# Kernel optimization log

Measured on AMD Instinct MI355X. Metric: run time of the kernel, lower is better.

The kernel has to match this reference:

```python
import jax, jax.numpy as jnp
import numpy as np

EMBED = 256
HEADS = 8
LEVELS = 4
POINTS = 4
HD = EMBED // HEADS  # 32
SHAPES = [(100, 100), (50, 50), (25, 25), (13, 13)]  # (H, W) per level
NV = sum(h * w for h, w in SHAPES)  # 13294
BS = 2


def _lin_params(k, fan_in, fan_out):
    s = 1.0 / np.sqrt(fan_in)
    kw, kb = jax.random.split(k)
    W = jax.random.uniform(kw, (fan_in, fan_out), jnp.float32, -s, s)
    b = jax.random.uniform(kb, (fan_out,), jnp.float32, -s, s)
    return W, b


def setup_inputs():
    key = jax.random.key(0)
    ks = jax.random.split(key, 10)
    inp = {
        "query": jax.random.normal(ks[0], (BS, NV, EMBED), jnp.float32),
        "key": jax.random.normal(ks[1], (BS, NV, EMBED), jnp.float32),
        "value": jax.random.normal(ks[2], (BS, NV, EMBED), jnp.float32),
        "query_pos": jax.random.normal(ks[3], (BS, NV, EMBED), jnp.float32),
        "reference_points": jax.random.uniform(ks[4], (BS, NV, LEVELS, 2), jnp.float32),
        "spatial_shapes": jnp.array(SHAPES, jnp.int32),
        "level_start_index": jnp.array(np.cumsum([0] + [h * w for h, w in SHAPES[:-1]]), jnp.int32),
        "key_padding_mask": jnp.zeros((BS, NV), bool),
    }
    inp["W_value"], inp["b_value"] = _lin_params(ks[5], EMBED, EMBED)
    inp["W_off"], inp["b_off"] = _lin_params(ks[6], EMBED, HEADS * LEVELS * POINTS * 2)
    inp["W_attn"], inp["b_attn"] = _lin_params(ks[7], EMBED, HEADS * LEVELS * POINTS)
    inp["W_out"], inp["b_out"] = _lin_params(ks[8], EMBED, EMBED)
    inp["W_ffn"], inp["b_ffn"] = _lin_params(ks[9], EMBED, EMBED)
    return inp


def _bilinear(v, x, y, H, W):
    # v: (bs, heads, H*W, hd); x, y: (bs, heads, n) pixel coords (align_corners=False)
    # zero padding outside the feature map (matches torch grid_sample padding_mode='zeros')
    x0 = jnp.floor(x)
    y0 = jnp.floor(y)
    lx = x - x0
    ly = y - y0
    x0 = x0.astype(jnp.int32)
    y0 = y0.astype(jnp.int32)

    def g(xi, yi):
        valid = ((xi >= 0) & (xi < W) & (yi >= 0) & (yi < H)).astype(v.dtype)
        idx = jnp.clip(yi, 0, H - 1) * W + jnp.clip(xi, 0, W - 1)
        return jnp.take_along_axis(v, idx[..., None], axis=2) * valid[..., None]

    return (g(x0, y0) * ((1 - lx) * (1 - ly))[..., None]
            + g(x0 + 1, y0) * (lx * (1 - ly))[..., None]
            + g(x0, y0 + 1) * ((1 - lx) * ly)[..., None]
            + g(x0 + 1, y0 + 1) * (lx * ly)[..., None])


def _forward(query, key, value, query_pos, reference_points, shapes, starts,
             key_padding_mask, W_value, b_value, W_off, b_off, W_attn, b_attn,
             W_out, b_out, W_ffn, b_ffn):
    bs, nq, _ = query.shape
    identity = query  # residual taken BEFORE adding positional encoding (mmcv semantics)
    q = query + query_pos
    v = value @ W_value + b_value
    v = jnp.where(key_padding_mask[..., None], 0.0, v).reshape(bs, -1, HEADS, HD)
    off = (q @ W_off + b_off).reshape(bs, nq, HEADS, LEVELS, POINTS, 2)
    aw = jax.nn.softmax((q @ W_attn + b_attn).reshape(bs, nq, HEADS, LEVELS * POINTS), axis=-1)
    aw = aw.reshape(bs, nq, HEADS, LEVELS, POINTS)
    # offset normalizer is (W, H) per level
    wh = jnp.array([[w, h] for h, w in shapes], jnp.float32)
    loc = reference_points[:, :, None, :, None, :] + off / wh[None, None, None, :, None, :]
    out = jnp.zeros((bs, HEADS, nq, HD), q.dtype)
    for l, (H, W) in enumerate(shapes):
        s = starts[l]
        vl = v[:, s:s + H * W].transpose(0, 2, 1, 3)  # (bs, heads, H*W, hd)
        x = (loc[:, :, :, l, :, 0] * W - 0.5).transpose(0, 2, 1, 3).reshape(bs, HEADS, nq * POINTS)
        y = (loc[:, :, :, l, :, 1] * H - 0.5).transpose(0, 2, 1, 3).reshape(bs, HEADS, nq * POINTS)
        smp = _bilinear(vl, x, y, H, W).reshape(bs, HEADS, nq, POINTS, HD)
        wl = aw[:, :, :, l].transpose(0, 2, 1, 3)  # (bs, heads, nq, P)
        out = out + jnp.sum(smp * wl[..., None], axis=3)
    out = out.transpose(0, 2, 1, 3).reshape(bs, nq, EMBED)
    out = out @ W_out + b_out + identity
    return out @ W_ffn + b_ffn


def reference(query, key, value, query_pos, reference_points, spatial_shapes,
              level_start_index, key_padding_mask, W_value, b_value, W_off, b_off,
              W_attn, b_attn, W_out, b_out, W_ffn, b_ffn):
    # spatial shapes / level starts are structural metadata -> treat as static ints
    shapes = [tuple(int(x) for x in r) for r in np.asarray(spatial_shapes)]
    starts = [int(x) for x in np.asarray(level_start_index)]
    return _forward(query, key, value, query_pos, reference_points, shapes, starts,
                    key_padding_mask, W_value, b_value, W_off, b_off, W_attn, b_attn,
                    W_out, b_out, W_ffn, b_ffn)
```

## Files before the change

### kernel.cpp

```cpp
#include <hip/hip_runtime.h>
#include <hip/hip_bf16.h>
#include <math.h>

#define NQ 13294
#define NV 13294
#define M_ROWS (2*NQ)
#define MP 26624

typedef __attribute__((ext_vector_type(8))) short bf16x8;
typedef __attribute__((ext_vector_type(4))) float f32x4;

__device__ __forceinline__ float4 ld4(const float* p){ return *(const float4*)p; }
__device__ __forceinline__ float bfu_lo(unsigned int u){ return __uint_as_float(u << 16); }
__device__ __forceinline__ float bfu_hi(unsigned int u){ return __uint_as_float(u & 0xffff0000u); }
__device__ __forceinline__ unsigned short f2bf(float f){
  unsigned int u = __float_as_uint(f);
  u += 0x7fffu + ((u >> 16) & 1u);
  return (unsigned short)(u >> 16);
}
__device__ __forceinline__ unsigned int pk2(float a, float b){
  return (unsigned int)f2bf(a) | ((unsigned int)f2bf(b) << 16);
}
__device__ __forceinline__ void gl_lds16(const unsigned short* g, unsigned short* l) {
  __builtin_amdgcn_global_load_lds(
      (const __attribute__((address_space(1))) unsigned int*)g,
      (__attribute__((address_space(3))) unsigned int*)l, 16, 0, 0);
}

__global__ __launch_bounds__(256) void prep_all(
    const float* __restrict__ value, const float* __restrict__ query,
    const float* __restrict__ qpos,
    unsigned short* __restrict__ val_bf, unsigned short* __restrict__ q_bf,
    const float* __restrict__ wv, const float* __restrict__ wo,
    const float* __restrict__ wa, const float* __restrict__ wu,
    const float* __restrict__ wf, unsigned short* __restrict__ wt)
{
  const int total = MP * 64;
  for (int i = blockIdx.x * 256 + threadIdx.x; i < total; i += gridDim.x * 256) {
    const int e = i * 4;
    ushort4 a = make_ushort4(0,0,0,0), b = make_ushort4(0,0,0,0);
    if (e < M_ROWS * 256) {
      float4 v4 = ld4(value + e);
      a = make_ushort4(f2bf(v4.x), f2bf(v4.y), f2bf(v4.z), f2bf(v4.w));
      float4 q4 = ld4(query + e);
      float4 p4 = ld4(qpos + e);
      b = make_ushort4(f2bf(q4.x+p4.x), f2bf(q4.y+p4.y), f2bf(q4.z+p4.z), f2bf(q4.w+p4.w));
    }
    *(ushort4*)(val_bf + e) = a;
    *(ushort4*)(q_bf   + e) = b;
  }
  for (int t = blockIdx.x * 256 + threadIdx.x; t < 294912; t += gridDim.x * 256) {
    const float* src; int Nn; int base;
    if      (t < 65536)  { src = wv; Nn = 256; base = 0; }
    else if (t < 131072) { src = wo; Nn = 256; base = 65536; }
    else if (t < 163840) { src = wa; Nn = 128; base = 131072; }
    else if (t < 229376) { src = wu; Nn = 256; base = 163840; }
    else                 { src = wf; Nn = 256; base = 229376; }
    const int local = t - base;
    const int n = local >> 8, k = local & 255;
    wt[t] = f2bf(src[k * Nn + n]);
  }
}

template<int NCOL, int OUT_MODE, bool ADD_RES>
__global__ __launch_bounds__(256) void gemm_gl(
    const unsigned short* __restrict__ A, const unsigned short* __restrict__ Bt,
    const float* __restrict__ biasA, const float* __restrict__ biasB,
    const float* __restrict__ RES, void* __restrict__ Cv, int N)
{
  __shared__ unsigned short lds[32768];

  const int nwg = 416 * NCOL;
  const int lin = blockIdx.x;
  const int swz = (lin & 7) * (nwg >> 3) + (lin >> 3);
  const int brow = (swz / NCOL) * 64;
  const int bcol = (swz % NCOL) * 64;

  const int tid  = threadIdx.x;
  const int wid  = tid >> 6, lane = tid & 63;
  const int wr   = wid >> 1, wc = wid & 1;
  const int fr   = lane & 15, fg = lane >> 4;

  {
    const int r0   = lane >> 3;
    const int slot = lane & 7;
    #pragma unroll
    for (int t = 0; t < 4; ++t) {
      #pragma unroll
      for (int c = 0; c < 2; ++c) {
        const int row = (wid * 2 + c) * 8 + r0;
        const int gsl = slot ^ (row & 7);
        gl_lds16(A  + (size_t)(brow + row) * 256 + t * 64 + (gsl << 3),
                 &lds[t * 4096 + (wid * 2 + c) * 512]);
        gl_lds16(Bt + (size_t)(bcol + row) * 256 + t * 64 + (gsl << 3),
                 &lds[16384 + t * 4096 + (wid * 2 + c) * 512]);
      }
    }
  }
  __syncthreads();

  f32x4 acc[2][2];
  #pragma unroll
  for (int m = 0; m < 2; ++m)
    #pragma unroll
    for (int n = 0; n < 2; ++n)
      acc[m][n] = (f32x4){0.f, 0.f, 0.f, 0.f};

  #pragma unroll
  for (int t = 0; t < 4; ++t) {
    const char* as = (const char*)&lds[t * 4096];
    const char* bs = (const char*)&lds[16384 + t * 4096];
    #pragma unroll
    for (int kk = 0; kk < 2; ++kk) {
      const int kb = kk * 64 + fg * 16;
      bf16x8 af[2], bfv[2];
      #pragma unroll
      for (int m = 0; m < 2; ++m) {
        const int r = wr * 32 + m * 16 + fr;
        af[m] = *(const bf16x8*)(as + r * 128 + (kb ^ ((r & 7) << 4)));
      }
      #pragma unroll
      for (int n = 0; n < 2; ++n) {
        const int r = wc * 32 + n * 16 + fr;
        bfv[n] = *(const bf16x8*)(bs + r * 128 + (kb ^ ((r & 7) << 4)));
      }
      #pragma unroll
      for (int m = 0; m < 2; ++m)
        #pragma unroll
        for (int n = 0; n < 2; ++n)
          acc[m][n] = __builtin_amdgcn_mfma_f32_16x16x32_bf16(af[m], bfv[n], acc[m][n], 0, 0, 0);
    }
  }

  __syncthreads();
  float* csh = (float*)lds;
  const int c0 = bcol + wc * 32 + fr;
  const int c1 = c0 + 16;
  const float bn0 = (c0 < 256) ? biasA[c0] : biasB[c0 - 256];
  const float bn1 = (c1 < 256) ? biasA[c1] : biasB[c1 - 256];
  #pragma unroll
  for (int m = 0; m < 2; ++m)
    #pragma unroll
    for (int j = 0; j < 4; ++j) {
      const int row = wr * 32 + m * 16 + fg * 4 + j;
      csh[row * 64 + wc * 32 + fr]      = acc[m][0][j] + bn0;
      csh[row * 64 + wc * 32 + 16 + fr] = acc[m][1][j] + bn1;
    }
  __syncthreads();
  #pragma unroll
  for (int i = 0; i < 4; ++i) {
    const int rl = i * 16 + (tid >> 4);
    const int gr = brow + rl;
    if (gr >= M_ROWS) continue;
    const int c4 = (tid & 15) * 4;
    float4 v = *(const float4*)&csh[rl * 64 + c4];
    if (ADD_RES) {
      float4 q = ld4(RES + (size_t)gr * 256 + bcol + c4);
      v.x += q.x; v.y += q.y; v.z += q.z; v.w += q.w;
    }
    if (OUT_MODE == 0) {
      *(float4*)&((float*)Cv)[(size_t)gr * N + bcol + c4] = v;
    } else if (OUT_MODE == 1) {
      ushort4 pk = make_ushort4(f2bf(v.x), f2bf(v.y), f2bf(v.z), f2bf(v.w));
      *(ushort4*)&((unsigned short*)Cv)[(size_t)gr * N + bcol + c4] = pk;
    } else {
      const int head = (bcol + c4) >> 5;
      const int ch   = c4 & 31;
      ushort4 pk = make_ushort4(f2bf(v.x), f2bf(v.y), f2bf(v.z), f2bf(v.w));
      *(ushort4*)&((unsigned short*)Cv)[((size_t)head * M_ROWS + gr) * 32 + ch] = pk;
    }
  }
}

__global__ __launch_bounds__(256) void msda5(
    const unsigned short* __restrict__ v, const unsigned short* __restrict__ oa,
    const float* __restrict__ ref, unsigned short* __restrict__ attout)
{
  constexpr int LW[4] = {100, 50, 25, 13};
  constexpr int LS[4] = {0, 10000, 12500, 13125};

  __shared__ int4   sidx[64][16];
  __shared__ float4 swt [64][16];

  const int bid   = blockIdx.x;
  const int h     = bid & 7;
  const int chunk = bid >> 3;
  const int tid   = threadIdx.x;
  const int qi    = tid >> 2;
  const int lq    = tid & 3;
  const int bq    = chunk * 64 + qi;
  const bool active = bq < M_ROWS;
  const int b     = (bq >= NQ) ? 1 : 0;
  const int pmask = qi & 7;

  if (active) {
    const int l = lq;
    const int W = LW[l];
    const float fD = (float)W;
    const unsigned short* oarow = oa + (size_t)bq * 384;

    uint2 lg = *(const uint2*)(oarow + 256 + h * 16 + l * 4);
    float g0 = bfu_lo(lg.x), g1 = bfu_hi(lg.x), g2 = bfu_lo(lg.y), g3 = bfu_hi(lg.y);
    float mx = fmaxf(fmaxf(g0, g1), fmaxf(g2, g3));
    mx = fmaxf(mx, __shfl_xor(mx, 1));
    mx = fmaxf(mx, __shfl_xor(mx, 2));
    float e0 = __expf(g0-mx), e1 = __expf(g1-mx), e2 = __expf(g2-mx), e3 = __expf(g3-mx);
    float s = e0 + e1 + e2 + e3;
    s += __shfl_xor(s, 1);
    s += __shfl_xor(s, 2);
    const float inv = 1.f / s;
    const float ee[4] = {e0*inv, e1*inv, e2*inv, e3*inv};

    uint4 ov = *(const uint4*)(oarow + h * 32 + l * 8);
    const float oxy[8] = {bfu_lo(ov.x), bfu_hi(ov.x), bfu_lo(ov.y), bfu_hi(ov.y),
                          bfu_lo(ov.z), bfu_hi(ov.z), bfu_lo(ov.w), bfu_hi(ov.w)};
    const float rx = ref[(size_t)bq * 8 + l * 2];
    const float ry = ref[(size_t)bq * 8 + l * 2 + 1];
    const int rowbase = b * NV + LS[l];

    #pragma unroll
    for (int j = 0; j < 4; ++j) {
      const float x = (rx + oxy[2*j]   / fD) * fD - 0.5f;
      const float y = (ry + oxy[2*j+1] / fD) * fD - 0.5f;
      const float x0f = floorf(x), y0f = floorf(y);
      const float lx = x - x0f, ly = y - y0f;
      const int x0 = (int)x0f, y0 = (int)y0f;
      const int x1 = x0 + 1,  y1 = y0 + 1;
      const int cx0 = min(max(x0, 0), W - 1), cx1 = min(max(x1, 0), W - 1);
      const int cy0 = min(max(y0, 0), W - 1), cy1 = min(max(y1, 0), W - 1);
      const float f00 = (x0 >= 0 && x0 < W && y0 >= 0 && y0 < W) ? 1.f : 0.f;
      const float f10 = (x1 >= 0 && x1 < W && y0 >= 0 && y0 < W) ? 1.f : 0.f;
      const float f01 = (x0 >= 0 && x0 < W && y1 >= 0 && y1 < W) ? 1.f : 0.f;
      const float f11 = (x1 >= 0 && x1 < W && y1 >= 0 && y1 < W) ? 1.f : 0.f;
      const float wt = ee[j];
      const int pi = (l * 4 + j) ^ pmask;
      sidx[qi][pi] = make_int4((rowbase + cy0 * W + cx0) * 64,
                               (rowbase + cy0 * W + cx1) * 64,
                               (rowbase + cy1 * W + cx0) * 64,
                               (rowbase + cy1 * W + cx1) * 64);
      swt[qi][pi] = make_float4(wt * (1.f - lx) * (1.f - ly) * f00,
                                wt * lx * (1.f - ly) * f10,
                                wt * (1.f - lx) * ly * f01,
                                wt * lx * ly * f11);
    }
  }
  __syncthreads();

  if (active) {
    const char* vb = (const char*)v + (size_t)h * M_ROWS * 64 + lq * 16;
    float acc[8] = {0.f, 0.f, 0.f, 0.f, 0.f, 0.f, 0.f, 0.f};
    #pragma unroll
    for (int p = 0; p < 16; ++p) {
      const int4   ix = sidx[qi][p ^ pmask];
      const float4 w4 = swt[qi][p ^ pmask];
      uint4 c0 = *(const uint4*)(vb + ix.x);
      uint4 c1 = *(const uint4*)(vb + ix.y);
      uint4 c2 = *(const uint4*)(vb + ix.z);
      uint4 c3 = *(const uint4*)(vb + ix.w);
      acc[0] = fmaf(w4.x, bfu_lo(c0.x), acc[0]); acc[1] = fmaf(w4.x, bfu_hi(c0.x), acc[1]);
      acc[2] = fmaf(w4.x, bfu_lo(c0.y), acc[2]); acc[3] = fmaf(w4.x, bfu_hi(c0.y), acc[3]);
      acc[4] = fmaf(w4.x, bfu_lo(c0.z), acc[4]); acc[5] = fmaf(w4.x, bfu_hi(c0.z), acc[5]);
      acc[6] = fmaf(w4.x, bfu_lo(c0.w), acc[6]); acc[7] = fmaf(w4.x, bfu_hi(c0.w), acc[7]);
      acc[0] = fmaf(w4.y, bfu_lo(c1.x), acc[0]); acc[1] = fmaf(w4.y, bfu_hi(c1.x), acc[1]);
      acc[2] = fmaf(w4.y, bfu_lo(c1.y), acc[2]); acc[3] = fmaf(w4.y, bfu_hi(c1.y), acc[3]);
      acc[4] = fmaf(w4.y, bfu_lo(c1.z), acc[4]); acc[5] = fmaf(w4.y, bfu_hi(c1.z), acc[5]);
      acc[6] = fmaf(w4.y, bfu_lo(c1.w), acc[6]); acc[7] = fmaf(w4.y, bfu_hi(c1.w), acc[7]);
      acc[0] = fmaf(w4.z, bfu_lo(c2.x), acc[0]); acc[1] = fmaf(w4.z, bfu_hi(c2.x), acc[1]);
      acc[2] = fmaf(w4.z, bfu_lo(c2.y), acc[2]); acc[3] = fmaf(w4.z, bfu_hi(c2.y), acc[3]);
      acc[4] = fmaf(w4.z, bfu_lo(c2.z), acc[4]); acc[5] = fmaf(w4.z, bfu_hi(c2.z), acc[5]);
      acc[6] = fmaf(w4.z, bfu_lo(c2.w), acc[6]); acc[7] = fmaf(w4.z, bfu_hi(c2.w), acc[7]);
      acc[0] = fmaf(w4.w, bfu_lo(c3.x), acc[0]); acc[1] = fmaf(w4.w, bfu_hi(c3.x), acc[1]);
      acc[2] = fmaf(w4.w, bfu_lo(c3.y), acc[2]); acc[3] = fmaf(w4.w, bfu_hi(c3.y), acc[3]);
      acc[4] = fmaf(w4.w, bfu_lo(c3.z), acc[4]); acc[5] = fmaf(w4.w, bfu_hi(c3.z), acc[5]);
      acc[6] = fmaf(w4.w, bfu_lo(c3.w), acc[6]); acc[7] = fmaf(w4.w, bfu_hi(c3.w), acc[7]);
    }
    uint4 pk;
    pk.x = pk2(acc[0], acc[1]);
    pk.y = pk2(acc[2], acc[3]);
    pk.z = pk2(acc[4], acc[5]);
    pk.w = pk2(acc[6], acc[7]);
    *(uint4*)(attout + (size_t)bq * 256 + h * 32 + lq * 8) = pk;
  }
}

extern "C" void kernel_launch(void* const* d_in, const int* in_sizes, int n_in,
                              void* d_out, int out_size, void* d_ws, size_t ws_size,
                              hipStream_t stream) {
  const float* query  = (const float*)d_in[0];
  const float* value  = (const float*)d_in[2];
  const float* qpos   = (const float*)d_in[3];
  const float* refpts = (const float*)d_in[4];
  const float* W_value = (const float*)d_in[8];
  const float* b_value = (const float*)d_in[9];
  const float* W_off   = (const float*)d_in[10];
  const float* b_off   = (const float*)d_in[11];
  const float* W_attn  = (const float*)d_in[12];
  const float* b_attn  = (const float*)d_in[13];
  const float* W_out   = (const float*)d_in[14];
  const float* b_out   = (const float*)d_in[15];
  const float* W_ffn   = (const float*)d_in[16];
  const float* b_ffn   = (const float*)d_in[17];
  float* out = (float*)d_out;

  unsigned short* oa    = (unsigned short*)d_ws;
  unsigned short* vbuf2 = oa + (size_t)MP * 384;
  unsigned short* AB1   = vbuf2 + (size_t)8 * M_ROWS * 32;
  unsigned short* AB2   = AB1 + (size_t)MP * 256;
  unsigned short* wts   = AB2 + (size_t)MP * 256;
  unsigned short* wv_t  = wts;
  unsigned short* woa_t = wts + 65536;
  unsigned short* wu_t  = wts + 163840;
  unsigned short* wf_t  = wts + 229376;

  const dim3 blk(256);

  prep_all<<<dim3(2048), blk, 0, stream>>>(value, query, qpos, AB1, AB2,
      W_value, W_off, W_attn, W_out, W_ffn, wts);

  gemm_gl<4,2,false><<<dim3(1664), blk, 0, stream>>>(
      AB1, wv_t, b_value, b_value, nullptr, vbuf2, 256);
  gemm_gl<6,1,false><<<dim3(2496), blk, 0, stream>>>(
      AB2, woa_t, b_off, b_attn, nullptr, oa, 384);
  msda5<<<dim3(8 * 416), blk, 0, stream>>>(vbuf2, oa, refpts, AB1);
  gemm_gl<4,1,true><<<dim3(1664), blk, 0, stream>>>(
      AB1, wu_t, b_out, b_out, query, AB2, 256);
  gemm_gl<4,0,false><<<dim3(1664), blk, 0, stream>>>(
      AB2, wf_t, b_ffn, b_ffn, nullptr, (void*)out, 256);
}
```

Before: 122.2 us.

## Fuse fp32-to-bf16 activation conversion into merged value/offset-attn GEMM

Activation conversion (value, and query plus query_pos) now happens inside the GEMM's A-tile load instead of in a separate prep pass that wrote bf16 copies. The value projection and the offset/attention projection also run in one launch, with blocks split by index. This removes a full write and re-read of two bf16 activation buffers and one launch. In exchange, A tiles are loaded from fp32 through registers rather than async global-to-LDS, and the N=256 value tiles are reread by 4 column blocks and the N=384 tiles by 6, so the fp32 reads and add are repeated per block.

```diff
diff --git a/kernel.cpp b/kernel.cpp
--- a/kernel.cpp
+++ b/kernel.cpp
@@ -27,46 +27,174 @@
       (__attribute__((address_space(3))) unsigned int*)l, 16, 0, 0);
 }
 
-__global__ __launch_bounds__(256) void prep_all(
-    const float* __restrict__ value, const float* __restrict__ query,
-    const float* __restrict__ qpos,
-    unsigned short* __restrict__ val_bf, unsigned short* __restrict__ q_bf,
+__global__ __launch_bounds__(256) void prep_w(
     const float* __restrict__ wv, const float* __restrict__ wo,
     const float* __restrict__ wa, const float* __restrict__ wu,
     const float* __restrict__ wf, unsigned short* __restrict__ wt)
 {
-  const int total = MP * 64;
-  for (int i = blockIdx.x * 256 + threadIdx.x; i < total; i += gridDim.x * 256) {
-    const int e = i * 4;
-    ushort4 a = make_ushort4(0,0,0,0), b = make_ushort4(0,0,0,0);
-    if (e < M_ROWS * 256) {
-      float4 v4 = ld4(value + e);
-      a = make_ushort4(f2bf(v4.x), f2bf(v4.y), f2bf(v4.z), f2bf(v4.w));
-      float4 q4 = ld4(query + e);
-      float4 p4 = ld4(qpos + e);
-      b = make_ushort4(f2bf(q4.x+p4.x), f2bf(q4.y+p4.y), f2bf(q4.z+p4.z), f2bf(q4.w+p4.w));
-    }
-    *(ushort4*)(val_bf + e) = a;
-    *(ushort4*)(q_bf   + e) = b;
-  }
-  for (int t = blockIdx.x * 256 + threadIdx.x; t < 294912; t += gridDim.x * 256) {
-    const float* src; int Nn; int base;
-    if      (t < 65536)  { src = wv; Nn = 256; base = 0; }
-    else if (t < 131072) { src = wo; Nn = 256; base = 65536; }
-    else if (t < 163840) { src = wa; Nn = 128; base = 131072; }
-    else if (t < 229376) { src = wu; Nn = 256; base = 163840; }
-    else                 { src = wf; Nn = 256; base = 229376; }
-    const int local = t - base;
-    const int n = local >> 8, k = local & 255;
-    wt[t] = f2bf(src[k * Nn + n]);
+  int t = blockIdx.x * 256 + threadIdx.x;
+  if (t >= 294912) return;
+  const float* src; int Nn; int base;
+  if      (t < 65536)  { src = wv; Nn = 256; base = 0; }
+  else if (t < 131072) { src = wo; Nn = 256; base = 65536; }
+  else if (t < 163840) { src = wa; Nn = 128; base = 131072; }
+  else if (t < 229376) { src = wu; Nn = 256; base = 163840; }
+  else                 { src = wf; Nn = 256; base = 229376; }
+  const int local = t - base;
+  const int n = local >> 8, k = local & 255;
+  wt[t] = f2bf(src[k * Nn + n]);
+}
+
+__global__ __launch_bounds__(256) void gemm_voa(
+    const float* __restrict__ value, const float* __restrict__ query,
+    const float* __restrict__ qpos,
+    const unsigned short* __restrict__ wv_t, const unsigned short* __restrict__ woa_t,
+    const float* __restrict__ b_value, const float* __restrict__ b_off,
+    const float* __restrict__ b_attn,
+    unsigned short* __restrict__ vbuf2, unsigned short* __restrict__ oa)
+{
+  __shared__ unsigned short lds[32768];
+
+  const bool is_v = blockIdx.x < 1664;
+  const int  ncol = is_v ? 4 : 6;
+  const int  lin  = is_v ? blockIdx.x : blockIdx.x - 1664;
+  const int  nwg  = is_v ? 1664 : 2496;
+  const int  N    = is_v ? 256 : 384;
+  const unsigned short* Bt = is_v ? wv_t : woa_t;
+
+  const int swz  = (lin & 7) * (nwg >> 3) + (lin >> 3);
+  const int brow = (swz / ncol) * 64;
+  const int bcol = (swz % ncol) * 64;
+
+  const int tid  = threadIdx.x;
+  const int wid  = tid >> 6, lane = tid & 63;
+  const int wr   = wid >> 1, wc = wid & 1;
+  const int fr   = lane & 15, fg = lane >> 4;
+
+  {
+    const int r0   = lane >> 3;
+    const int slot = lane & 7;
+    #pragma unroll
+    for (int t = 0; t < 4; ++t) {
+      #pragma unroll
+      for (int c = 0; c < 2; ++c) {
+        const int row = (wid * 2 + c) * 8 + r0;
+        const int gsl = slot ^ (row & 7);
+        gl_lds16(Bt + (size_t)(bcol + row) * 256 + t * 64 + (gsl << 3),
+                 &lds[16384 + t * 4096 + (wid * 2 + c) * 512]);
+      }
+    }
+  }
+  {
+    const int srow = tid >> 3;
+    const int slot = tid & 7;
+    const int ke0  = slot << 3;
+    #pragma unroll
+    for (int t = 0; t < 4; ++t) {
+      #pragma unroll
+      for (int c = 0; c < 2; ++c) {
+        const int row = c * 32 + srow;
+        const int gr  = brow + row;
+        const int ke  = t * 64 + ke0;
+        float4 f0 = make_float4(0.f,0.f,0.f,0.f), f1 = f0;
+        if (gr < M_ROWS) {
+          if (is_v) {
+            f0 = ld4(value + (size_t)gr * 256 + ke);
+            f1 = ld4(value + (size_t)gr * 256 + ke + 4);
+          } else {
+            f0 = ld4(query + (size_t)gr * 256 + ke);
+            f1 = ld4(query + (size_t)gr * 256 + ke + 4);
+            float4 g0 = ld4(qpos + (size_t)gr * 256 + ke);
+            float4 g1 = ld4(qpos + (size_t)gr * 256 + ke + 4);
+            f0.x += g0.x; f0.y += g0.y; f0.z += g0.z; f0.w += g0.w;
+            f1.x += g1.x; f1.y += g1.y; f1.z += g1.z; f1.w += g1.w;
+          }
+        }
+        uint4 pk;
+        pk.x = pk2(f0.x, f0.y); pk.y = pk2(f0.z, f0.w);
+        pk.z = pk2(f1.x, f1.y); pk.w = pk2(f1.z, f1.w);
+        const int sw = slot ^ (row & 7);
+        *(uint4*)((char*)&lds[t * 4096] + row * 128 + (sw << 4)) = pk;
+      }
+    }
+  }
+  __syncthreads();
+
+  f32x4 acc[2][2];
+  #pragma unroll
+  for (int m = 0; m < 2; ++m)
+    #pragma unroll
+    for (int n = 0; n < 2; ++n)
+      acc[m][n] = (f32x4){0.f, 0.f, 0.f, 0.f};
+
+  #pragma unroll
+  for (int t = 0; t < 4; ++t) {
+    const char* as = (const char*)&lds[t * 4096];
+    const char* bs = (const char*)&lds[16384 + t * 4096];
+    #pragma unroll
+    for (int kk = 0; kk < 2; ++kk) {
+      const int kb = kk * 64 + fg * 16;
+      bf16x8 af[2], bfv[2];
+      #pragma unroll
+      for (int m = 0; m < 2; ++m) {
+        const int r = wr * 32 + m * 16 + fr;
+        af[m] = *(const bf16x8*)(as + r * 128 + (kb ^ ((r & 7) << 4)));
+      }
+      #pragma unroll
+      for (int n = 0; n < 2; ++n) {
+        const int r = wc * 32 + n * 16 + fr;
+        bfv[n] = *(const bf16x8*)(bs + r * 128 + (kb ^ ((r & 7) << 4)));
+      }
+      #pragma unroll
+      for (int m = 0; m < 2; ++m)
+        #pragma unroll
+        for (int n = 0; n < 2; ++n)
+          acc[m][n] = __builtin_amdgcn_mfma_f32_16x16x32_bf16(af[m], bfv[n], acc[m][n], 0, 0, 0);
+    }
+  }
+
+  __syncthreads();
+  float* csh = (float*)lds;
+  const int c0 = bcol + wc * 32 + fr;
+  const int c1 = c0 + 16;
+  float bn0, bn1;
+  if (is_v) { bn0 = b_value[c0]; bn1 = b_value[c1]; }
+  else {
+    bn0 = (c0 < 256) ? b_off[c0] : b_attn[c0 - 256];
+    bn1 = (c1 < 256) ? b_off[c1] : b_attn[c1 - 256];
+  }
+  #pragma unroll
+  for (int m = 0; m < 2; ++m)
+    #pragma unroll
+    for (int j = 0; j < 4; ++j) {
+      const int row = wr * 32 + m * 16 + fg * 4 + j;
+      csh[row * 64 + wc * 32 + fr]      = acc[m][0][j] + bn0;
+      csh[row * 64 + wc * 32 + 16 + fr] = acc[m][1][j] + bn1;
+    }
+  __syncthreads();
+  #pragma unroll
+  for (int i = 0; i < 4; ++i) {
+    const int rl = i * 16 + (tid >> 4);
+    const int gr = brow + rl;
+    if (gr >= M_ROWS) continue;
+    const int c4 = (tid & 15) * 4;
+    float4 v = *(const float4*)&csh[rl * 64 + c4];
+    ushort4 pk = make_ushort4(f2bf(v.x), f2bf(v.y), f2bf(v.z), f2bf(v.w));
+    if (is_v) {
+      const int head = (bcol + c4) >> 5;
+      const int ch   = c4 & 31;
+      *(ushort4*)&vbuf2[((size_t)head * M_ROWS + gr) * 32 + ch] = pk;
+    } else {
+      *(ushort4*)&oa[(size_t)gr * 384 + bcol + c4] = pk;
+    }
   }
 }
 
 template<int NCOL, int OUT_MODE, bool ADD_RES>
 __global__ __launch_bounds__(256) void gemm_gl(
     const unsigned short* __restrict__ A, const unsigned short* __restrict__ Bt,
-    const float* __restrict__ biasA, const float* __restrict__ biasB,
-    const float* __restrict__ RES, void* __restrict__ Cv, int N)
+    const float* __restrict__ bias, const float* __restrict__ RES,
+    void* __restrict__ Cv, int N)
 {
   __shared__ unsigned short lds[32768];
 
@@ -136,8 +264,8 @@
   float* csh = (float*)lds;
   const int c0 = bcol + wc * 32 + fr;
   const int c1 = c0 + 16;
-  const float bn0 = (c0 < 256) ? biasA[c0] : biasB[c0 - 256];
-  const float bn1 = (c1 < 256) ? biasA[c1] : biasB[c1 - 256];
+  const float bn0 = bias[c0];
+  const float bn1 = bias[c1];
   #pragma unroll
   for (int m = 0; m < 2; ++m)
     #pragma unroll
@@ -160,14 +288,9 @@
     }
     if (OUT_MODE == 0) {
       *(float4*)&((float*)Cv)[(size_t)gr * N + bcol + c4] = v;
-    } else if (OUT_MODE == 1) {
+    } else {
       ushort4 pk = make_ushort4(f2bf(v.x), f2bf(v.y), f2bf(v.z), f2bf(v.w));
       *(ushort4*)&((unsigned short*)Cv)[(size_t)gr * N + bcol + c4] = pk;
-    } else {
-      const int head = (bcol + c4) >> 5;
-      const int ch   = c4 & 31;
-      ushort4 pk = make_ushort4(f2bf(v.x), f2bf(v.y), f2bf(v.z), f2bf(v.w));
-      *(ushort4*)&((unsigned short*)Cv)[((size_t)head * M_ROWS + gr) * 32 + ch] = pk;
     }
   }
 }
@@ -314,16 +437,13 @@
 
   const dim3 blk(256);
 
-  prep_all<<<dim3(2048), blk, 0, stream>>>(value, query, qpos, AB1, AB2,
-      W_value, W_off, W_attn, W_out, W_ffn, wts);
-
-  gemm_gl<4,2,false><<<dim3(1664), blk, 0, stream>>>(
-      AB1, wv_t, b_value, b_value, nullptr, vbuf2, 256);
-  gemm_gl<6,1,false><<<dim3(2496), blk, 0, stream>>>(
-      AB2, woa_t, b_off, b_attn, nullptr, oa, 384);
+  prep_w<<<dim3(1152), blk, 0, stream>>>(W_value, W_off, W_attn, W_out, W_ffn, wts);
+
+  gemm_voa<<<dim3(1664 + 2496), blk, 0, stream>>>(
+      value, query, qpos, wv_t, woa_t, b_value, b_off, b_attn, vbuf2, oa);
   msda5<<<dim3(8 * 416), blk, 0, stream>>>(vbuf2, oa, refpts, AB1);
   gemm_gl<4,1,true><<<dim3(1664), blk, 0, stream>>>(
-      AB1, wu_t, b_out, b_out, query, AB2, 256);
+      AB1, wu_t, b_out, query, AB2, 256);
   gemm_gl<4,0,false><<<dim3(1664), blk, 0, stream>>>(
-      AB2, wf_t, b_ffn, b_ffn, nullptr, (void*)out, 256);
-}
+      AB2, wf_t, b_ffn, nullptr, (void*)out, 256);
+}
```

Result: slower. 133.6 us (+9.4%).
